# Optimization experiments

Hardware: AMD Instinct MI355X
Metric: run time of the kernel (lower is better)

Reference implementation:

```python
import jax, jax.numpy as jnp
import numpy as np

N = 50000
E = 800000
IN_C, HID, OUT_C, HEADS = 128, 16, 64, 4
NEG_SLOPE = 0.2


def _gat_conv(x, src, dst, W, a_src, a_dst, b, heads, concat):
    # x: [N, Fin]; W: [Fin, heads*Fout]; a_src/a_dst: [heads, Fout]; b: [out]
    n = x.shape[0]
    h = (x @ W).reshape(n, heads, -1)                      # [N, H, F]
    alpha_s = jnp.einsum('nhf,hf->nh', h, a_src)           # [N, H]
    alpha_d = jnp.einsum('nhf,hf->nh', h, a_dst)
    e = jax.nn.leaky_relu(alpha_s[src] + alpha_d[dst], NEG_SLOPE)  # [E, H]
    m = jax.ops.segment_max(e, dst, num_segments=n)        # per-dest max (self-loops ensure nonempty)
    w = jnp.exp(e - m[dst])
    denom = jax.ops.segment_sum(w, dst, num_segments=n)
    alpha = w / (denom[dst] + 1e-16)                       # [E, H] segment softmax
    out = jax.ops.segment_sum(h[src] * alpha[:, :, None], dst, num_segments=n)  # [N, H, F]
    out = out.reshape(n, -1) if concat else out.mean(axis=1)
    return out + b


def setup_inputs() -> dict:
    key = jax.random.key(0)
    ks = jax.random.split(key, 16)
    x = jax.random.normal(ks[0], (N, IN_C), dtype=jnp.float32)
    edge_index = jax.random.randint(ks[1], (2, E), 0, N, dtype=jnp.int64)
    s = 0.1
    d = {'x': x, 'edge_index': edge_index}
    # layer 0: in=128 -> heads=4, F=16
    d['W0'] = jax.random.normal(ks[2], (IN_C, HEADS * HID), dtype=jnp.float32) * s
    d['as0'] = jax.random.normal(ks[3], (HEADS, HID), dtype=jnp.float32) * s
    d['ad0'] = jax.random.normal(ks[4], (HEADS, HID), dtype=jnp.float32) * s
    d['b0'] = jnp.zeros((HEADS * HID,), dtype=jnp.float32)
    # layer 1: in=64 -> heads=4, F=16
    d['W1'] = jax.random.normal(ks[5], (HEADS * HID, HEADS * HID), dtype=jnp.float32) * s
    d['as1'] = jax.random.normal(ks[6], (HEADS, HID), dtype=jnp.float32) * s
    d['ad1'] = jax.random.normal(ks[7], (HEADS, HID), dtype=jnp.float32) * s
    d['b1'] = jnp.zeros((HEADS * HID,), dtype=jnp.float32)
    # layer 2: in=64 -> heads=1, F=64, concat=False
    d['W2'] = jax.random.normal(ks[8], (HEADS * HID, OUT_C), dtype=jnp.float32) * s
    d['as2'] = jax.random.normal(ks[9], (1, OUT_C), dtype=jnp.float32) * s
    d['ad2'] = jax.random.normal(ks[10], (1, OUT_C), dtype=jnp.float32) * s
    d['b2'] = jnp.zeros((OUT_C,), dtype=jnp.float32)
    return d


def reference(x, edge_index, W0, as0, ad0, b0, W1, as1, ad1, b1, W2, as2, ad2, b2):
    loops = jnp.arange(N, dtype=edge_index.dtype)
    src = jnp.concatenate([edge_index[0], loops])  # PyG add_self_loops=True
    dst = jnp.concatenate([edge_index[1], loops])
    h = _gat_conv(x, src, dst, W0, as0, ad0, b0, HEADS, True)
    h = jax.nn.elu(h)
    h = _gat_conv(h, src, dst, W1, as1, ad1, b1, HEADS, True)
    h = jax.nn.elu(h)
    return _gat_conv(h, src, dst, W2, as2, ad2, b2, 1, False)
```

## Files before the change

kernel.cpp:

```cpp
#include <hip/hip_runtime.h>
#include <hip/hip_bf16.h>
#include <math.h>


#define NEG_SLOPE 0.2f
#define L1_CHUNK 4096


__global__ __launch_bounds__(256) void k_l1hist(
    const int* __restrict__ idx, int* __restrict__ ghist, int E, int etot) {
    __shared__ int h[256];
    const int t = threadIdx.x;
    h[t] = 0;
    __syncthreads();
    const int base = blockIdx.x * L1_CHUNK;
    for (int i = t; i < L1_CHUNK; i += 256) {
        int e = base + i;
        if (e >= etot) break;
        int dst = (e < E) ? idx[E + e] : (e - E);
        atomicAdd(&h[dst >> 8], 1);
    }
    __syncthreads();
    if (h[t]) atomicAdd(&ghist[t], h[t]);
}

__global__ __launch_bounds__(256) void k_scan256(
    const int* __restrict__ ghist, int* __restrict__ goff, int* __restrict__ gcur) {
    __shared__ int sc[256];
    const int t = threadIdx.x;
    int v = ghist[t];
    sc[t] = v;
    __syncthreads();
    for (int o = 1; o < 256; o <<= 1) {
        int x = (t >= o) ? sc[t - o] : 0;
        __syncthreads();
        sc[t] += x;
        __syncthreads();
    }
    int excl = sc[t] - v;
    goff[t] = excl;
    gcur[t] = excl;
    if (t == 255) goff[256] = sc[255];
}

__global__ __launch_bounds__(256) void k_l1scatter(
    const int* __restrict__ idx, int* __restrict__ gcur,
    unsigned long long* __restrict__ buf, int E, int etot) {
    __shared__ int h[256];
    __shared__ int lbase[256];
    const int t = threadIdx.x;
    h[t] = 0;
    __syncthreads();
    const int base = blockIdx.x * L1_CHUNK;
    for (int i = t; i < L1_CHUNK; i += 256) {
        int e = base + i;
        if (e >= etot) break;
        int dst = (e < E) ? idx[E + e] : (e - E);
        atomicAdd(&h[dst >> 8], 1);
    }
    __syncthreads();
    lbase[t] = h[t] ? atomicAdd(&gcur[t], h[t]) : 0;
    __syncthreads();
    h[t] = lbase[t];
    __syncthreads();
    for (int i = t; i < L1_CHUNK; i += 256) {
        int e = base + i;
        if (e >= etot) break;
        int dst, src;
        if (e < E) { dst = idx[E + e]; src = idx[e]; }
        else       { dst = src = e - E; }
        int pos = atomicAdd(&h[dst >> 8], 1);
        buf[pos] = ((unsigned long long)(unsigned)dst << 32) | (unsigned)src;
    }
}

__global__ __launch_bounds__(256) void k_l2build(
    const unsigned long long* __restrict__ buf, const int* __restrict__ goff,
    int* __restrict__ off, int* __restrict__ csr, int n, int etot) {
    __shared__ int sc[256];
    __shared__ int lcur[256];
    const int b = blockIdx.x, t = threadIdx.x;
    const int lo = goff[b], hi = goff[b + 1];
    sc[t] = 0;
    __syncthreads();
    for (int p = lo + t; p < hi; p += 256) {
        int dst = (int)(buf[p] >> 32);
        atomicAdd(&sc[dst & 255], 1);
    }
    __syncthreads();
    int v = sc[t];
    __syncthreads();
    sc[t] = v;
    __syncthreads();
    for (int o = 1; o < 256; o <<= 1) {
        int x = (t >= o) ? sc[t - o] : 0;
        __syncthreads();
        sc[t] += x;
        __syncthreads();
    }
    int excl = sc[t] - v;
    const int d = b * 256 + t;
    if (d < n) off[d] = lo + excl;
    lcur[t] = lo + excl;
    __syncthreads();
    for (int p = lo + t; p < hi; p += 256) {
        unsigned long long e = buf[p];
        int dst = (int)(e >> 32);
        int src = (int)(e & 0xffffffffu);
        int pos = atomicAdd(&lcur[dst & 255], 1);
        csr[pos] = src;
    }
    if (b == 0 && t == 0) off[n] = etot;
}


template <int K, int H, int F>
__global__ __launch_bounds__(256) void k_gemm_alpha(
    const float* __restrict__ x, const float* __restrict__ W,
    const float* __restrict__ a_s, const float* __restrict__ a_d,
    float* __restrict__ h, float* __restrict__ as_o, float* __restrict__ ad_o,
    int n) {
    __shared__ float xs[16][K];
    const int tid = threadIdx.x;
    const int base = blockIdx.x * 16;
    int rows = n - base; if (rows > 16) rows = 16;
    const int kv = K / 4;
    for (int i = tid; i < rows * kv; i += 256) {
        int r = i / kv, c = i - r * kv;
        ((float4*)&xs[r][0])[c] = ((const float4*)(x + (size_t)(base + r) * K))[c];
    }
    __syncthreads();
    const int w = tid >> 6, lane = tid & 63;
    const int node0 = base + w * 4;
    float acc0 = 0.f, acc1 = 0.f, acc2 = 0.f, acc3 = 0.f;
    #pragma unroll 4
    for (int k = 0; k < K; ++k) {
        float wv = W[k * 64 + lane];
        acc0 = fmaf(xs[w * 4 + 0][k], wv, acc0);
        acc1 = fmaf(xs[w * 4 + 1][k], wv, acc1);
        acc2 = fmaf(xs[w * 4 + 2][k], wv, acc2);
        acc3 = fmaf(xs[w * 4 + 3][k], wv, acc3);
    }
    const int head = (H == 1) ? 0 : (lane >> 4);
    const int f = (H == 1) ? lane : (lane & (F - 1));
    const float asv = a_s[head * F + f];
    const float adv = a_d[head * F + f];
    float accs[4] = {acc0, acc1, acc2, acc3};
    #pragma unroll
    for (int j = 0; j < 4; ++j) {
        int node = node0 + j;
        if (node >= n) break;
        h[(size_t)node * 64 + lane] = accs[j];
        float vs = accs[j] * asv;
        float vd = accs[j] * adv;
        #pragma unroll
        for (int o = F >> 1; o > 0; o >>= 1) {
            vs += __shfl_xor(vs, o);
            vd += __shfl_xor(vd, o);
        }
        if (f == 0) {
            as_o[node * H + head] = vs;
            ad_o[node * H + head] = vd;
        }
    }
}

template <int H, bool ELU>
__global__ __launch_bounds__(256) void k_agg(
    const float* __restrict__ h, const float* __restrict__ as_b,
    const float* __restrict__ ad_b, const int* __restrict__ off,
    const int* __restrict__ csr, const float* __restrict__ bias,
    float* __restrict__ out, int n) {
    const int w = threadIdx.x >> 6, lane = threadIdx.x & 63;
    const int node = blockIdx.x * 4 + w;
    if (node >= n) return;
    const int q = lane >> 4;
    const int c4 = lane & 15;
    const int head = (H == 1) ? 0 : (c4 >> 2);
    const float ad_n = ad_b[node * H + head];
    const int b = off[node], e = off[node + 1];
    float m = -1e30f, den = 0.f;
    float4 acc = {0.f, 0.f, 0.f, 0.f};
    int p = b + q;
    int s_cur = 0; float as_cur = 0.f;
    if (p < e) {
        s_cur = csr[p];
        as_cur = as_b[s_cur * H + head];
    }
    while (p < e) {
        const int pn = p + 4;
        int s_nxt = 0; float as_nxt = 0.f;
        if (pn < e) {
            s_nxt = csr[pn];
            as_nxt = as_b[s_nxt * H + head];
        }
        float ev = as_cur + ad_n;
        ev = ev > 0.f ? ev : NEG_SLOPE * ev;
        float mn = fmaxf(m, ev);
        float sc = __expf(m - mn);
        float wv = __expf(ev - mn);
        m = mn;
        const float4 hv = *(const float4*)(h + (size_t)s_cur * 64 + c4 * 4);
        den = fmaf(den, sc, wv);
        acc.x = fmaf(acc.x, sc, wv * hv.x);
        acc.y = fmaf(acc.y, sc, wv * hv.y);
        acc.z = fmaf(acc.z, sc, wv * hv.z);
        acc.w = fmaf(acc.w, sc, wv * hv.w);
        p = pn; s_cur = s_nxt; as_cur = as_nxt;
    }
    float m2 = fmaxf(m, __shfl_xor(m, 16));
    float mt = fmaxf(m2, __shfl_xor(m2, 32));
    float sc = __expf(m - mt);
    den *= sc; acc.x *= sc; acc.y *= sc; acc.z *= sc; acc.w *= sc;
    den += __shfl_xor(den, 16); den += __shfl_xor(den, 32);
    acc.x += __shfl_xor(acc.x, 16); acc.x += __shfl_xor(acc.x, 32);
    acc.y += __shfl_xor(acc.y, 16); acc.y += __shfl_xor(acc.y, 32);
    acc.z += __shfl_xor(acc.z, 16); acc.z += __shfl_xor(acc.z, 32);
    acc.w += __shfl_xor(acc.w, 16); acc.w += __shfl_xor(acc.w, 32);
    if (q == 0) {
        float inv = 1.f / (den + 1e-16f);
        float4 r;
        r.x = acc.x * inv + bias[c4 * 4 + 0];
        r.y = acc.y * inv + bias[c4 * 4 + 1];
        r.z = acc.z * inv + bias[c4 * 4 + 2];
        r.w = acc.w * inv + bias[c4 * 4 + 3];
        if (ELU) {
            r.x = r.x > 0.f ? r.x : expm1f(r.x);
            r.y = r.y > 0.f ? r.y : expm1f(r.y);
            r.z = r.z > 0.f ? r.z : expm1f(r.z);
            r.w = r.w > 0.f ? r.w : expm1f(r.w);
        }
        *(float4*)(out + (size_t)node * 64 + c4 * 4) = r;
    }
}


extern "C" void kernel_launch(void* const* d_in, const int* in_sizes, int n_in,
                              void* d_out, int out_size, void* d_ws, size_t ws_size,
                              hipStream_t stream) {
    const float* x   = (const float*)d_in[0];
    const int*   idx = (const int*)d_in[1];
    const float* W0  = (const float*)d_in[2];
    const float* as0 = (const float*)d_in[3];
    const float* ad0 = (const float*)d_in[4];
    const float* b0  = (const float*)d_in[5];
    const float* W1  = (const float*)d_in[6];
    const float* as1 = (const float*)d_in[7];
    const float* ad1 = (const float*)d_in[8];
    const float* b1  = (const float*)d_in[9];
    const float* W2  = (const float*)d_in[10];
    const float* as2 = (const float*)d_in[11];
    const float* ad2 = (const float*)d_in[12];
    const float* b2  = (const float*)d_in[13];
    float* out = (float*)d_out;

    const int n    = in_sizes[0] / 128;
    const int E    = in_sizes[1] / 2;
    const int etot = E + n;

    char* p = (char*)d_ws;
    auto alloc = [&](size_t bytes) {
        char* r = p;
        p += (bytes + 255) & ~(size_t)255;
        return r;
    };
    int*   off   = (int*)alloc((size_t)(n + 1) * 4);
    int*   csr   = (int*)alloc((size_t)etot * 4);
    int*   ghist = (int*)alloc(256 * 4);
    int*   goff  = (int*)alloc(257 * 4);
    int*   gcur  = (int*)alloc(256 * 4);
    float* asb   = (float*)alloc((size_t)n * 4 * 4);
    float* adb   = (float*)alloc((size_t)n * 4 * 4);
    float* hA    = (float*)alloc((size_t)n * 64 * 4);
    unsigned long long* buf = (unsigned long long*)hA;

    const int nb_l1 = (etot + L1_CHUNK - 1) / L1_CHUNK;
    const int nb_l2 = (n + 255) / 256;
    const int nb_g  = (n + 15) / 16;
    const int nb_w  = (n + 3) / 4;

    hipMemsetAsync(ghist, 0, 256 * 4, stream);
    k_l1hist<<<nb_l1, 256, 0, stream>>>(idx, ghist, E, etot);
    k_scan256<<<1, 256, 0, stream>>>(ghist, goff, gcur);
    k_l1scatter<<<nb_l1, 256, 0, stream>>>(idx, gcur, buf, E, etot);
    k_l2build<<<nb_l2, 256, 0, stream>>>(buf, goff, off, csr, n, etot);

    k_gemm_alpha<128, 4, 16><<<nb_g, 256, 0, stream>>>(x, W0, as0, ad0, hA, asb, adb, n);
    k_agg<4, true><<<nb_w, 256, 0, stream>>>(hA, asb, adb, off, csr, b0, out, n);

    k_gemm_alpha<64, 4, 16><<<nb_g, 256, 0, stream>>>(out, W1, as1, ad1, hA, asb, adb, n);
    k_agg<4, true><<<nb_w, 256, 0, stream>>>(hA, asb, adb, off, csr, b1, out, n);

    k_gemm_alpha<64, 1, 64><<<nb_g, 256, 0, stream>>>(out, W2, as2, ad2, hA, asb, adb, n);
    k_agg<1, false><<<nb_w, 256, 0, stream>>>(hA, asb, adb, off, csr, b2, out, n);
}
```

Measured before the change: 319.9 us.

## Fuse GAT aggregation with next layer GEMM and drop online softmax max

Each aggregation kernel for layers 0 and 1 now also applies bias and ELU, stages the result in shared memory, and runs the next layer's 64x64 projection plus attention-logit reductions in the same kernel. This removes two launches and the global round trip of the intermediate activations, using ping-pong buffers for h and the alpha arrays. The edge loop also drops the running-max rescaling and exponentiates logits directly, which saves exps and multiplies but risks overflow for large logits. Each wave now processes four nodes serially, which may reduce latency hiding in the gather.

```diff
diff --git a/kernel.cpp b/kernel.cpp
--- a/kernel.cpp
+++ b/kernel.cpp
@@ -113,6 +113,43 @@
     if (b == 0 && t == 0) off[n] = etot;
 }
 
+
+template <int H>
+__device__ __forceinline__ float4 agg_node(
+    const float* __restrict__ h, const float* __restrict__ asb,
+    const float* __restrict__ adb, const int* __restrict__ off,
+    const int* __restrict__ csr, int node, int q, int c4) {
+    const int head = (H == 1) ? 0 : (c4 >> 2);
+    const float ad_n = adb[node * H + head];
+    const int b = off[node], e = off[node + 1];
+    float den = 0.f;
+    float4 acc = {0.f, 0.f, 0.f, 0.f};
+    int p = b + q;
+    int s_cur = 0; float as_cur = 0.f;
+    if (p < e) { s_cur = csr[p]; as_cur = asb[s_cur * H + head]; }
+    while (p < e) {
+        const int pn = p + 4;
+        int s_nxt = 0; float as_nxt = 0.f;
+        if (pn < e) { s_nxt = csr[pn]; as_nxt = asb[s_nxt * H + head]; }
+        float ev = as_cur + ad_n;
+        ev = ev > 0.f ? ev : NEG_SLOPE * ev;
+        float wv = __expf(ev);
+        const float4 hv = *(const float4*)(h + (size_t)s_cur * 64 + c4 * 4);
+        den += wv;
+        acc.x = fmaf(wv, hv.x, acc.x);
+        acc.y = fmaf(wv, hv.y, acc.y);
+        acc.z = fmaf(wv, hv.z, acc.z);
+        acc.w = fmaf(wv, hv.w, acc.w);
+        p = pn; s_cur = s_nxt; as_cur = as_nxt;
+    }
+    den += __shfl_xor(den, 16); den += __shfl_xor(den, 32);
+    acc.x += __shfl_xor(acc.x, 16); acc.x += __shfl_xor(acc.x, 32);
+    acc.y += __shfl_xor(acc.y, 16); acc.y += __shfl_xor(acc.y, 32);
+    acc.z += __shfl_xor(acc.z, 16); acc.z += __shfl_xor(acc.z, 32);
+    acc.w += __shfl_xor(acc.w, 16); acc.w += __shfl_xor(acc.w, 32);
+    float inv = 1.f / (den + 1e-16f);
+    return make_float4(acc.x * inv, acc.y * inv, acc.z * inv, acc.w * inv);
+}
 
 template <int K, int H, int F>
 __global__ __launch_bounds__(256) void k_gemm_alpha(
@@ -165,71 +202,83 @@
     }
 }
 
-template <int H, bool ELU>
-__global__ __launch_bounds__(256) void k_agg(
-    const float* __restrict__ h, const float* __restrict__ as_b,
-    const float* __restrict__ ad_b, const int* __restrict__ off,
+template <int HA, int HG, int FG>
+__global__ __launch_bounds__(256) void k_agg_gemm(
+    const float* __restrict__ h_in, const float* __restrict__ asb_in,
+    const float* __restrict__ adb_in, const int* __restrict__ off,
+    const int* __restrict__ csr, const float* __restrict__ bias,
+    const float* __restrict__ W, const float* __restrict__ a_s,
+    const float* __restrict__ a_d, float* __restrict__ h_out,
+    float* __restrict__ asb_out, float* __restrict__ adb_out, int n) {
+    __shared__ float xs[16][64];
+    const int tid = threadIdx.x;
+    const int w = tid >> 6, lane = tid & 63;
+    const int q = lane >> 4, c4 = lane & 15;
+    const int base = blockIdx.x * 16;
+    #pragma unroll
+    for (int j = 0; j < 4; ++j) {
+        const int node = base + w * 4 + j;
+        if (node < n) {
+            float4 r = agg_node<HA>(h_in, asb_in, adb_in, off, csr, node, q, c4);
+            if (q == 0) {
+                r.x += bias[c4 * 4 + 0]; r.y += bias[c4 * 4 + 1];
+                r.z += bias[c4 * 4 + 2]; r.w += bias[c4 * 4 + 3];
+                r.x = r.x > 0.f ? r.x : expm1f(r.x);
+                r.y = r.y > 0.f ? r.y : expm1f(r.y);
+                r.z = r.z > 0.f ? r.z : expm1f(r.z);
+                r.w = r.w > 0.f ? r.w : expm1f(r.w);
+                *(float4*)&xs[w * 4 + j][c4 * 4] = r;
+            }
+        }
+    }
+    __syncthreads();
+    float acc0 = 0.f, acc1 = 0.f, acc2 = 0.f, acc3 = 0.f;
+    #pragma unroll 4
+    for (int k = 0; k < 64; ++k) {
+        float wv = W[k * 64 + lane];
+        acc0 = fmaf(xs[w * 4 + 0][k], wv, acc0);
+        acc1 = fmaf(xs[w * 4 + 1][k], wv, acc1);
+        acc2 = fmaf(xs[w * 4 + 2][k], wv, acc2);
+        acc3 = fmaf(xs[w * 4 + 3][k], wv, acc3);
+    }
+    const int head = (HG == 1) ? 0 : (lane >> 4);
+    const int f = (HG == 1) ? lane : (lane & (FG - 1));
+    const float asv = a_s[head * FG + f];
+    const float adv = a_d[head * FG + f];
+    float accs[4] = {acc0, acc1, acc2, acc3};
+    const int node0 = base + w * 4;
+    #pragma unroll
+    for (int j = 0; j < 4; ++j) {
+        int node = node0 + j;
+        if (node >= n) break;
+        h_out[(size_t)node * 64 + lane] = accs[j];
+        float vs = accs[j] * asv;
+        float vd = accs[j] * adv;
+        #pragma unroll
+        for (int o = FG >> 1; o > 0; o >>= 1) {
+            vs += __shfl_xor(vs, o);
+            vd += __shfl_xor(vd, o);
+        }
+        if (f == 0) {
+            asb_out[node * HG + head] = vs;
+            adb_out[node * HG + head] = vd;
+        }
+    }
+}
+
+__global__ __launch_bounds__(256) void k_agg_final(
+    const float* __restrict__ h, const float* __restrict__ asb,
+    const float* __restrict__ adb, const int* __restrict__ off,
     const int* __restrict__ csr, const float* __restrict__ bias,
     float* __restrict__ out, int n) {
     const int w = threadIdx.x >> 6, lane = threadIdx.x & 63;
     const int node = blockIdx.x * 4 + w;
     if (node >= n) return;
-    const int q = lane >> 4;
-    const int c4 = lane & 15;
-    const int head = (H == 1) ? 0 : (c4 >> 2);
-    const float ad_n = ad_b[node * H + head];
-    const int b = off[node], e = off[node + 1];
-    float m = -1e30f, den = 0.f;
-    float4 acc = {0.f, 0.f, 0.f, 0.f};
-    int p = b + q;
-    int s_cur = 0; float as_cur = 0.f;
-    if (p < e) {
-        s_cur = csr[p];
-        as_cur = as_b[s_cur * H + head];
-    }
-    while (p < e) {
-        const int pn = p + 4;
-        int s_nxt = 0; float as_nxt = 0.f;
-        if (pn < e) {
-            s_nxt = csr[pn];
-            as_nxt = as_b[s_nxt * H + head];
-        }
-        float ev = as_cur + ad_n;
-        ev = ev > 0.f ? ev : NEG_SLOPE * ev;
-        float mn = fmaxf(m, ev);
-        float sc = __expf(m - mn);
-        float wv = __expf(ev - mn);
-        m = mn;
-        const float4 hv = *(const float4*)(h + (size_t)s_cur * 64 + c4 * 4);
-        den = fmaf(den, sc, wv);
-        acc.x = fmaf(acc.x, sc, wv * hv.x);
-        acc.y = fmaf(acc.y, sc, wv * hv.y);
-        acc.z = fmaf(acc.z, sc, wv * hv.z);
-        acc.w = fmaf(acc.w, sc, wv * hv.w);
-        p = pn; s_cur = s_nxt; as_cur = as_nxt;
-    }
-    float m2 = fmaxf(m, __shfl_xor(m, 16));
-    float mt = fmaxf(m2, __shfl_xor(m2, 32));
-    float sc = __expf(m - mt);
-    den *= sc; acc.x *= sc; acc.y *= sc; acc.z *= sc; acc.w *= sc;
-    den += __shfl_xor(den, 16); den += __shfl_xor(den, 32);
-    acc.x += __shfl_xor(acc.x, 16); acc.x += __shfl_xor(acc.x, 32);
-    acc.y += __shfl_xor(acc.y, 16); acc.y += __shfl_xor(acc.y, 32);
-    acc.z += __shfl_xor(acc.z, 16); acc.z += __shfl_xor(acc.z, 32);
-    acc.w += __shfl_xor(acc.w, 16); acc.w += __shfl_xor(acc.w, 32);
+    const int q = lane >> 4, c4 = lane & 15;
+    float4 r = agg_node<1>(h, asb, adb, off, csr, node, q, c4);
     if (q == 0) {
-        float inv = 1.f / (den + 1e-16f);
-        float4 r;
-        r.x = acc.x * inv + bias[c4 * 4 + 0];
-        r.y = acc.y * inv + bias[c4 * 4 + 1];
-        r.z = acc.z * inv + bias[c4 * 4 + 2];
-        r.w = acc.w * inv + bias[c4 * 4 + 3];
-        if (ELU) {
-            r.x = r.x > 0.f ? r.x : expm1f(r.x);
-            r.y = r.y > 0.f ? r.y : expm1f(r.y);
-            r.z = r.z > 0.f ? r.z : expm1f(r.z);
-            r.w = r.w > 0.f ? r.w : expm1f(r.w);
-        }
+        r.x += bias[c4 * 4 + 0]; r.y += bias[c4 * 4 + 1];
+        r.z += bias[c4 * 4 + 2]; r.w += bias[c4 * 4 + 3];
         *(float4*)(out + (size_t)node * 64 + c4 * 4) = r;
     }
 }
@@ -269,10 +318,13 @@
     int*   ghist = (int*)alloc(256 * 4);
     int*   goff  = (int*)alloc(257 * 4);
     int*   gcur  = (int*)alloc(256 * 4);
-    float* asb   = (float*)alloc((size_t)n * 4 * 4);
-    float* adb   = (float*)alloc((size_t)n * 4 * 4);
+    float* asbA  = (float*)alloc((size_t)n * 4 * 4);
+    float* adbA  = (float*)alloc((size_t)n * 4 * 4);
+    float* asbB  = (float*)alloc((size_t)n * 4 * 4);
+    float* adbB  = (float*)alloc((size_t)n * 4 * 4);
     float* hA    = (float*)alloc((size_t)n * 64 * 4);
-    unsigned long long* buf = (unsigned long long*)hA;
+    float* hB    = (float*)alloc((size_t)n * 64 * 4);
+    unsigned long long* buf = (unsigned long long*)hB;
 
     const int nb_l1 = (etot + L1_CHUNK - 1) / L1_CHUNK;
     const int nb_l2 = (n + 255) / 256;
@@ -285,12 +337,10 @@
     k_l1scatter<<<nb_l1, 256, 0, stream>>>(idx, gcur, buf, E, etot);
     k_l2build<<<nb_l2, 256, 0, stream>>>(buf, goff, off, csr, n, etot);
 
-    k_gemm_alpha<128, 4, 16><<<nb_g, 256, 0, stream>>>(x, W0, as0, ad0, hA, asb, adb, n);
-    k_agg<4, true><<<nb_w, 256, 0, stream>>>(hA, asb, adb, off, csr, b0, out, n);
-
-    k_gemm_alpha<64, 4, 16><<<nb_g, 256, 0, stream>>>(out, W1, as1, ad1, hA, asb, adb, n);
-    k_agg<4, true><<<nb_w, 256, 0, stream>>>(hA, asb, adb, off, csr, b1, out, n);
-
-    k_gemm_alpha<64, 1, 64><<<nb_g, 256, 0, stream>>>(out, W2, as2, ad2, hA, asb, adb, n);
-    k_agg<1, false><<<nb_w, 256, 0, stream>>>(hA, asb, adb, off, csr, b2, out, n);
-}
+    k_gemm_alpha<128, 4, 16><<<nb_g, 256, 0, stream>>>(x, W0, as0, ad0, hA, asbA, adbA, n);
+    k_agg_gemm<4, 4, 16><<<nb_g, 256, 0, stream>>>(hA, asbA, adbA, off, csr, b0,
+                                                   W1, as1, ad1, hB, asbB, adbB, n);
+    k_agg_gemm<4, 1, 64><<<nb_g, 256, 0, stream>>>(hB, asbB, adbB, off, csr, b1,
+                                                   W2, as2, ad2, hA, asbA, adbA, n);
+    k_agg_final<<<nb_w, 256, 0, stream>>>(hA, asbA, adbA, off, csr, b2, out, n);
+}
```

After: 302.5 us. 5.4% less time.
